# Optimization experiments

Hardware: AMD Instinct MI355X
Metric: run time of the kernel (lower is better)

The kernel has to match this reference:

```python
import math
import jax, jax.numpy as jnp
import numpy as np

D_MODEL = 1024
HEADS = 16
B, S = 4, 2048


def setup_inputs() -> dict:
    key = jax.random.key(0)
    ks = jax.random.split(key, 8)
    scale = 1.0 / math.sqrt(D_MODEL)
    return {
        "q": jax.random.normal(ks[0], (B, S, D_MODEL), dtype=jnp.float32),
        "k": jax.random.normal(ks[1], (B, S, D_MODEL), dtype=jnp.float32),
        "v": jax.random.normal(ks[2], (B, S, D_MODEL), dtype=jnp.float32),
        "mask": jax.random.randint(ks[3], (B, S), 0, 2).astype(jnp.bool_),
        "alibi_mask": jax.random.normal(ks[4], (1, HEADS, S, S), dtype=jnp.float32),
        "Wq": jax.random.normal(ks[5], (D_MODEL, D_MODEL), dtype=jnp.float32) * scale,
        "Wk": jax.random.normal(ks[6], (D_MODEL, D_MODEL), dtype=jnp.float32) * scale,
        "Wv": jax.random.normal(ks[7], (D_MODEL, D_MODEL), dtype=jnp.float32) * scale,
    }


def _split_heads(x):
    b, s, d = x.shape
    return x.reshape(b, s, HEADS, d // HEADS).transpose(0, 2, 1, 3)  # [B,H,S,hd]


def reference(q, k, v, mask, alibi_mask, Wq, Wk, Wv):
    # QKV projections (Linear, no bias)
    qh = _split_heads(q @ Wq)
    kh = _split_heads(k @ Wk)
    vh = _split_heads(v @ Wv)
    depth = qh.shape[-1]
    # naive full attention matrix [B,H,Sq,Sk]
    w = jnp.einsum("bhqd,bhkd->bhqk", qh, kh) / math.sqrt(depth)
    # mask: [B,Sk] -> [B,1,1,Sk], True = masked
    w = jnp.where(mask[:, None, None, :], -jnp.inf, w)
    w = w + alibi_mask
    a = jax.nn.softmax(w, axis=-1)  # dropout p=0 -> identity
    out = jnp.einsum("bhqk,bhkd->bhqd", a, vh)
    # combine heads -> [B,S,D]
    out = out.transpose(0, 2, 1, 3).reshape(q.shape[0], q.shape[1], -1)
    return (out, a)
```

## Files before the change

### kernel.cpp

```cpp
#include <hip/hip_runtime.h>
#include <hip/hip_bf16.h>
#include <math.h>

constexpr int B  = 4;
constexpr int S  = 2048;
constexpr int D  = 1024;
constexpr int H  = 16;
constexpr int HD = 64;
constexpr float SCALE = 0.125f;

using f32x4 = __attribute__((ext_vector_type(4))) float;
using s16x8 = __attribute__((ext_vector_type(8))) short;
using u16x8 = __attribute__((ext_vector_type(8))) unsigned short;
using u16x4 = __attribute__((ext_vector_type(4))) unsigned short;

__device__ __forceinline__ unsigned short f2bf(float f) {
    union { float f; unsigned u; } x; x.f = f;
    unsigned r = x.u + 0x7fffu + ((x.u >> 16) & 1u);
    return (unsigned short)(r >> 16);
}
__device__ __forceinline__ float bf2f(unsigned short h) {
    union { unsigned u; float f; } x; x.u = ((unsigned)h) << 16;
    return x.f;
}

#define MFMA_BF16(Af, Bf, Cf) __builtin_amdgcn_mfma_f32_16x16x32_bf16(Af, Bf, Cf, 0, 0, 0)

__global__ __launch_bounds__(256) void k_wt(const float* __restrict__ W,
                                            unsigned short* __restrict__ Wt) {
    __shared__ unsigned short T[64][68];
    const int k0 = blockIdx.x * 64, n0 = blockIdx.y * 64;
    const int t = threadIdx.x;
    {
        const int kr = t >> 4, nc4 = (t & 15) * 4;
        for (int rr = 0; rr < 4; ++rr) {
            const int kk = kr + rr * 16;
            f32x4 wv = *reinterpret_cast<const f32x4*>(&W[(size_t)(k0 + kk) * D + n0 + nc4]);
#pragma unroll
            for (int j = 0; j < 4; ++j) T[nc4 + j][kk] = f2bf(wv[j]);
        }
    }
    __syncthreads();
    {
        const int nr = t >> 4, kc4 = (t & 15) * 4;
        for (int rr = 0; rr < 4; ++rr) {
            const int nn = nr + rr * 16;
            u16x4 o;
#pragma unroll
            for (int j = 0; j < 4; ++j) o[j] = T[nn][kc4 + j];
            *reinterpret_cast<u16x4*>(&Wt[(size_t)(n0 + nn) * D + k0 + kc4]) = o;
        }
    }
}

__global__ __launch_bounds__(256) void k_proj_mfma(const float* __restrict__ X,
                                                   const unsigned short* __restrict__ Wt,
                                                   unsigned short* __restrict__ Y) {
    __shared__ alignas(16) unsigned short As[128][72];
    __shared__ alignas(16) unsigned short Bs[128][72];
    const int bm = blockIdx.y * 128, bn = blockIdx.x * 128;
    const int t = threadIdx.x, w = t >> 6, l = t & 63;
    const int wr = w >> 1, wc = w & 1;
    const int lr = l & 15, lg = l >> 4;
    f32x4 acc[4][4] = {};

    for (int k0 = 0; k0 < D; k0 += 64) {
        {
            const int c4 = (t & 15) * 4;
            int row = t >> 4;
            for (int rr = 0; rr < 8; ++rr, row += 16) {
                f32x4 xv = *reinterpret_cast<const f32x4*>(&X[(size_t)(bm + row) * D + k0 + c4]);
                u16x4 hv;
#pragma unroll
                for (int j = 0; j < 4; ++j) hv[j] = f2bf(xv[j]);
                *reinterpret_cast<u16x4*>(&As[row][c4]) = hv;
            }
        }
        for (int i = 0; i < 4; ++i) {
            const int idx = t + i * 256;
            const int row = idx >> 3, c8 = (idx & 7) * 8;
            *reinterpret_cast<u16x8*>(&Bs[row][c8]) =
                *reinterpret_cast<const u16x8*>(&Wt[(size_t)(bn + row) * D + k0 + c8]);
        }
        __syncthreads();
#pragma unroll
        for (int kk = 0; kk < 2; ++kk) {
            s16x8 af[4], bf[4];
#pragma unroll
            for (int f = 0; f < 4; ++f) {
                af[f] = *reinterpret_cast<const s16x8*>(&As[wr * 64 + f * 16 + lr][kk * 32 + lg * 8]);
                bf[f] = *reinterpret_cast<const s16x8*>(&Bs[wc * 64 + f * 16 + lr][kk * 32 + lg * 8]);
            }
#pragma unroll
            for (int fm = 0; fm < 4; ++fm)
#pragma unroll
                for (int fn = 0; fn < 4; ++fn)
                    acc[fm][fn] = MFMA_BF16(af[fm], bf[fn], acc[fm][fn]);
        }
        __syncthreads();
    }
#pragma unroll
    for (int fm = 0; fm < 4; ++fm)
#pragma unroll
        for (int fn = 0; fn < 4; ++fn)
#pragma unroll
            for (int r = 0; r < 4; ++r) {
                const int m = bm + wr * 64 + fm * 16 + lg * 4 + r;
                const int n = bn + wc * 64 + fn * 16 + lr;
                const int b = m >> 11, s = m & (S - 1);
                const int h = n >> 6, e = n & 63;
                Y[(((size_t)(b * H + h) * S) + s) * HD + e] = f2bf(acc[fm][fn][r]);
            }
}

__global__ __launch_bounds__(256) void k_vt(const unsigned short* __restrict__ Vh,
                                            unsigned short* __restrict__ VT) {
    __shared__ alignas(16) unsigned short T[64][264];
    const int bh = blockIdx.y;
    const int s0 = blockIdx.x * 256;
    const int t = threadIdx.x;
    {
        const int e4 = (t & 15) * 4;
        int sr = t >> 4;
        for (int rr = 0; rr < 16; ++rr, sr += 16) {
            u16x4 vv = *reinterpret_cast<const u16x4*>(&Vh[((size_t)bh * S + s0 + sr) * HD + e4]);
#pragma unroll
            for (int j = 0; j < 4; ++j) T[e4 + j][sr] = vv[j];
        }
    }
    __syncthreads();
    {
        const int e = t >> 2, sl0 = (t & 3) * 64;
        for (int c = 0; c < 8; ++c) {
            u16x8 o = *reinterpret_cast<const u16x8*>(&T[e][sl0 + c * 8]);
            *reinterpret_cast<u16x8*>(&VT[((size_t)bh * HD + e) * S + s0 + sl0 + c * 8]) = o;
        }
    }
}

__global__ __launch_bounds__(256) void k_abf16(const float* __restrict__ A,
                                               unsigned short* __restrict__ O) {
    const size_t N = (size_t)H * S * S;
    const size_t stride = (size_t)gridDim.x * 256 * 8;
    for (size_t i = ((size_t)blockIdx.x * 256 + threadIdx.x) * 8; i < N; i += stride) {
        f32x4 a0 = *reinterpret_cast<const f32x4*>(&A[i]);
        f32x4 a1 = *reinterpret_cast<const f32x4*>(&A[i + 4]);
        u16x8 o;
#pragma unroll
        for (int j = 0; j < 4; ++j) { o[j] = f2bf(a0[j]); o[4 + j] = f2bf(a1[j]); }
        *reinterpret_cast<u16x8*>(&O[i]) = o;
    }
}

template <bool ABF16>
__global__ __launch_bounds__(512, 4) void k_fused(
    const unsigned short* __restrict__ QH, const unsigned short* __restrict__ KH,
    const unsigned short* __restrict__ VT, const float* __restrict__ ALIBI,
    const unsigned short* __restrict__ ABF, const int* __restrict__ MASK,
    float* __restrict__ Aout, float* __restrict__ OUT) {
    __shared__ alignas(16) unsigned short Qs[128][72];
    __shared__ alignas(16) unsigned short Ks[64][72];
    __shared__ alignas(16) unsigned short Vs[64][72];
    __shared__ alignas(16) unsigned short ALs[128][72];
    __shared__ alignas(16) unsigned short Ps[128][72];

    const int bh = blockIdx.y, b = bh >> 4, h = bh & 15;
    const int q0 = blockIdx.x * 128;
    const int t = threadIdx.x, w = t >> 6, ln = t & 63;
    const int lr = ln & 15, lg = ln >> 4;
    const unsigned short NEGBIG = f2bf(-1e30f);

    const unsigned short* Qb = QH + (size_t)bh * S * HD;
    const unsigned short* Kb = KH + (size_t)bh * S * HD;
    const unsigned short* Vb = VT + (size_t)bh * HD * S;
    const size_t hoff = (size_t)h * S * S;

#pragma unroll
    for (int i = 0; i < 2; ++i) {
        const int idx = t + i * 512, row = idx >> 3, c8 = (idx & 7) * 8;
        *reinterpret_cast<u16x8*>(&Qs[row][c8]) =
            *reinterpret_cast<const u16x8*>(&Qb[(size_t)(q0 + row) * HD + c8]);
    }
    __syncthreads();
    s16x8 qf[2];
#pragma unroll
    for (int kk = 0; kk < 2; ++kk)
        qf[kk] = *reinterpret_cast<const s16x8*>(&Qs[w * 16 + lr][kk * 32 + lg * 8]);

    float psum[4] = {0.f, 0.f, 0.f, 0.f};

    for (int k0 = 0; k0 < S; k0 += 64) {
        {
            const int row = t >> 3, c8 = (t & 7) * 8;
            *reinterpret_cast<u16x8*>(&Ks[row][c8]) =
                *reinterpret_cast<const u16x8*>(&Kb[(size_t)(k0 + row) * HD + c8]);
        }
#pragma unroll
        for (int i = 0; i < 2; ++i) {
            const int idx = t + i * 512, row = idx >> 3, c8 = (idx & 7) * 8;
            int4 m0 = *reinterpret_cast<const int4*>(&MASK[b * S + k0 + c8]);
            int4 m1 = *reinterpret_cast<const int4*>(&MASK[b * S + k0 + c8 + 4]);
            u16x8 av;
            if constexpr (ABF16) {
                av = *reinterpret_cast<const u16x8*>(&ABF[hoff + (size_t)(q0 + row) * S + k0 + c8]);
            } else {
                f32x4 a0 = *reinterpret_cast<const f32x4*>(&ALIBI[hoff + (size_t)(q0 + row) * S + k0 + c8]);
                f32x4 a1 = *reinterpret_cast<const f32x4*>(&ALIBI[hoff + (size_t)(q0 + row) * S + k0 + c8 + 4]);
#pragma unroll
                for (int j = 0; j < 4; ++j) { av[j] = f2bf(a0[j]); av[4 + j] = f2bf(a1[j]); }
            }
            u16x8 sv;
            sv[0] = m0.x ? NEGBIG : av[0];
            sv[1] = m0.y ? NEGBIG : av[1];
            sv[2] = m0.z ? NEGBIG : av[2];
            sv[3] = m0.w ? NEGBIG : av[3];
            sv[4] = m1.x ? NEGBIG : av[4];
            sv[5] = m1.y ? NEGBIG : av[5];
            sv[6] = m1.z ? NEGBIG : av[6];
            sv[7] = m1.w ? NEGBIG : av[7];
            *reinterpret_cast<u16x8*>(&ALs[row][c8]) = sv;
        }
        __syncthreads();

        f32x4 acc[4] = {};
#pragma unroll
        for (int kk = 0; kk < 2; ++kk)
#pragma unroll
            for (int fn = 0; fn < 4; ++fn) {
                s16x8 kf = *reinterpret_cast<const s16x8*>(&Ks[fn * 16 + lr][kk * 32 + lg * 8]);
                acc[fn] = MFMA_BF16(qf[kk], kf, acc[fn]);
            }
#pragma unroll
        for (int r = 0; r < 4; ++r) {
            const int rowl = w * 16 + lg * 4 + r;
            float s = 0.f;
#pragma unroll
            for (int fn = 0; fn < 4; ++fn)
                s += __expf(fmaf(acc[fn][r], SCALE, bf2f(ALs[rowl][fn * 16 + lr])));
            psum[r] += s;
        }
        __syncthreads();
    }

    float invl[4];
#pragma unroll
    for (int r = 0; r < 4; ++r) {
        float ps = psum[r];
#pragma unroll
        for (int off = 1; off < 16; off <<= 1) ps += __shfl_xor(ps, off, 64);
        invl[r] = 1.0f / ps;
    }

    f32x4 oacc[4] = {};
    for (int k0 = 0; k0 < S; k0 += 64) {
        {
            const int row = t >> 3, c8 = (t & 7) * 8;
            *reinterpret_cast<u16x8*>(&Ks[row][c8]) =
                *reinterpret_cast<const u16x8*>(&Kb[(size_t)(k0 + row) * HD + c8]);
            *reinterpret_cast<u16x8*>(&Vs[row][c8]) =
                *reinterpret_cast<const u16x8*>(&Vb[(size_t)row * S + k0 + c8]);
        }
#pragma unroll
        for (int i = 0; i < 2; ++i) {
            const int idx = t + i * 512, row = idx >> 3, c8 = (idx & 7) * 8;
            int4 m0 = *reinterpret_cast<const int4*>(&MASK[b * S + k0 + c8]);
            int4 m1 = *reinterpret_cast<const int4*>(&MASK[b * S + k0 + c8 + 4]);
            u16x8 av;
            if constexpr (ABF16) {
                av = *reinterpret_cast<const u16x8*>(&ABF[hoff + (size_t)(q0 + row) * S + k0 + c8]);
            } else {
                f32x4 a0 = *reinterpret_cast<const f32x4*>(&ALIBI[hoff + (size_t)(q0 + row) * S + k0 + c8]);
                f32x4 a1 = *reinterpret_cast<const f32x4*>(&ALIBI[hoff + (size_t)(q0 + row) * S + k0 + c8 + 4]);
#pragma unroll
                for (int j = 0; j < 4; ++j) { av[j] = f2bf(a0[j]); av[4 + j] = f2bf(a1[j]); }
            }
            u16x8 sv;
            sv[0] = m0.x ? NEGBIG : av[0];
            sv[1] = m0.y ? NEGBIG : av[1];
            sv[2] = m0.z ? NEGBIG : av[2];
            sv[3] = m0.w ? NEGBIG : av[3];
            sv[4] = m1.x ? NEGBIG : av[4];
            sv[5] = m1.y ? NEGBIG : av[5];
            sv[6] = m1.z ? NEGBIG : av[6];
            sv[7] = m1.w ? NEGBIG : av[7];
            *reinterpret_cast<u16x8*>(&ALs[row][c8]) = sv;
        }
        __syncthreads();

        f32x4 acc[4] = {};
#pragma unroll
        for (int kk = 0; kk < 2; ++kk)
#pragma unroll
            for (int fn = 0; fn < 4; ++fn) {
                s16x8 kf = *reinterpret_cast<const s16x8*>(&Ks[fn * 16 + lr][kk * 32 + lg * 8]);
                acc[fn] = MFMA_BF16(qf[kk], kf, acc[fn]);
            }
#pragma unroll
        for (int r = 0; r < 4; ++r) {
            const int rowl = w * 16 + lg * 4 + r;
#pragma unroll
            for (int fn = 0; fn < 4; ++fn) {
                float p = __expf(fmaf(acc[fn][r], SCALE, bf2f(ALs[rowl][fn * 16 + lr]))) * invl[r];
                Ps[rowl][fn * 16 + lr] = f2bf(p);
            }
        }
        __syncthreads();

#pragma unroll
        for (int i = 0; i < 2; ++i) {
            const int idx = t + i * 512, row = idx >> 3, sub = idx & 7;
            u16x8 pv = *reinterpret_cast<const u16x8*>(&Ps[row][sub * 8]);
            f32x4 o0, o1;
#pragma unroll
            for (int j = 0; j < 4; ++j) { o0[j] = bf2f(pv[j]); o1[j] = bf2f(pv[4 + j]); }
            float* dst = &Aout[((size_t)bh * S + q0 + row) * S + k0 + sub * 8];
            *reinterpret_cast<f32x4*>(dst) = o0;
            *reinterpret_cast<f32x4*>(dst + 4) = o1;
        }
#pragma unroll
        for (int c = 0; c < 2; ++c) {
            s16x8 pa = *reinterpret_cast<const s16x8*>(&Ps[w * 16 + lr][c * 32 + lg * 8]);
#pragma unroll
            for (int fn = 0; fn < 4; ++fn) {
                s16x8 vf = *reinterpret_cast<const s16x8*>(&Vs[fn * 16 + lr][c * 32 + lg * 8]);
                oacc[fn] = MFMA_BF16(pa, vf, oacc[fn]);
            }
        }
        __syncthreads();
    }

#pragma unroll
    for (int fn = 0; fn < 4; ++fn)
#pragma unroll
        for (int r = 0; r < 4; ++r)
            OUT[(size_t)(b * S + q0 + w * 16 + lg * 4 + r) * D + h * HD + fn * 16 + lr] =
                oacc[fn][r];
}

extern "C" void kernel_launch(void* const* d_in, const int* in_sizes, int n_in,
                              void* d_out, int out_size, void* d_ws, size_t ws_size,
                              hipStream_t stream) {
    const float* q     = (const float*)d_in[0];
    const float* k     = (const float*)d_in[1];
    const float* v     = (const float*)d_in[2];
    const int*   mask  = (const int*)d_in[3];
    const float* alibi = (const float*)d_in[4];
    const float* Wq    = (const float*)d_in[5];
    const float* Wk    = (const float*)d_in[6];
    const float* Wv    = (const float*)d_in[7];

    float* out = (float*)d_out;
    float* a   = out + (size_t)B * S * D;

    const size_t NH = (size_t)B * H * S * HD;
    unsigned short* qh  = (unsigned short*)d_ws;
    unsigned short* kh  = qh + NH;
    unsigned short* vh  = kh + NH;
    unsigned short* vT  = vh + NH;
    unsigned short* wqt = vT + NH;
    unsigned short* wkt = wqt + (size_t)D * D;
    unsigned short* wvt = wkt + (size_t)D * D;
    unsigned short* abf = wvt + (size_t)D * D;

    const size_t need_bf16 = ((size_t)(abf - qh) + (size_t)H * S * S) * sizeof(unsigned short);
    const bool use_abf16 = ws_size >= need_bf16;

    const dim3 blk(256);

    k_wt<<<dim3(D / 64, D / 64), blk, 0, stream>>>(Wq, wqt);
    k_wt<<<dim3(D / 64, D / 64), blk, 0, stream>>>(Wk, wkt);
    k_wt<<<dim3(D / 64, D / 64), blk, 0, stream>>>(Wv, wvt);

    if (use_abf16)
        k_abf16<<<dim3(8192), blk, 0, stream>>>(alibi, abf);

    k_proj_mfma<<<dim3(D / 128, (B * S) / 128), blk, 0, stream>>>(q, wqt, qh);
    k_proj_mfma<<<dim3(D / 128, (B * S) / 128), blk, 0, stream>>>(k, wkt, kh);
    k_proj_mfma<<<dim3(D / 128, (B * S) / 128), blk, 0, stream>>>(v, wvt, vh);

    k_vt<<<dim3(S / 256, B * H), blk, 0, stream>>>(vh, vT);

    if (use_abf16)
        k_fused<true><<<dim3(S / 128, B * H), dim3(512), 0, stream>>>(
            qh, kh, vT, alibi, abf, mask, a, out);
    else
        k_fused<false><<<dim3(S / 128, B * H), dim3(512), 0, stream>>>(
            qh, kh, vT, alibi, abf, mask, a, out);
}
```

Baseline: 714.3 us.

## Split fused attention into sum-exp and output kernels with per-column mask add

The single fused kernel is split into two launches: one computes the softmax denominators and writes inverse row sums to a workspace buffer, and the other recomputes scores, writes the probability matrix and accumulates the output. Each kernel uses less LDS (no Q tile; the sum kernel also drops the V and P tiles) and loads Q fragments straight from global memory. Masking changes from per-element selects while staging the alibi tile to a per-lane additive term read once per column. The intent is to raise occupancy and cut LDS and staging work, at the cost of an extra launch and a small global round trip for the inverse sums.

After: 714.3 us. No clear change (-0.0%).

```diff
diff --git a/kernel.cpp b/kernel.cpp
--- a/kernel.cpp
+++ b/kernel.cpp
@@ -153,39 +153,27 @@
 }
 
 template <bool ABF16>
-__global__ __launch_bounds__(512, 4) void k_fused(
+__global__ __launch_bounds__(512, 4) void k_sumexp(
     const unsigned short* __restrict__ QH, const unsigned short* __restrict__ KH,
-    const unsigned short* __restrict__ VT, const float* __restrict__ ALIBI,
-    const unsigned short* __restrict__ ABF, const int* __restrict__ MASK,
-    float* __restrict__ Aout, float* __restrict__ OUT) {
-    __shared__ alignas(16) unsigned short Qs[128][72];
+    const float* __restrict__ ALIBI, const unsigned short* __restrict__ ABF,
+    const int* __restrict__ MASK, float* __restrict__ INVL) {
     __shared__ alignas(16) unsigned short Ks[64][72];
-    __shared__ alignas(16) unsigned short Vs[64][72];
     __shared__ alignas(16) unsigned short ALs[128][72];
-    __shared__ alignas(16) unsigned short Ps[128][72];
 
     const int bh = blockIdx.y, b = bh >> 4, h = bh & 15;
     const int q0 = blockIdx.x * 128;
     const int t = threadIdx.x, w = t >> 6, ln = t & 63;
     const int lr = ln & 15, lg = ln >> 4;
-    const unsigned short NEGBIG = f2bf(-1e30f);
 
     const unsigned short* Qb = QH + (size_t)bh * S * HD;
     const unsigned short* Kb = KH + (size_t)bh * S * HD;
-    const unsigned short* Vb = VT + (size_t)bh * HD * S;
     const size_t hoff = (size_t)h * S * S;
 
-#pragma unroll
-    for (int i = 0; i < 2; ++i) {
-        const int idx = t + i * 512, row = idx >> 3, c8 = (idx & 7) * 8;
-        *reinterpret_cast<u16x8*>(&Qs[row][c8]) =
-            *reinterpret_cast<const u16x8*>(&Qb[(size_t)(q0 + row) * HD + c8]);
-    }
-    __syncthreads();
     s16x8 qf[2];
 #pragma unroll
     for (int kk = 0; kk < 2; ++kk)
-        qf[kk] = *reinterpret_cast<const s16x8*>(&Qs[w * 16 + lr][kk * 32 + lg * 8]);
+        qf[kk] = *reinterpret_cast<const s16x8*>(
+            &Qb[(size_t)(q0 + w * 16 + lr) * HD + kk * 32 + lg * 8]);
 
     float psum[4] = {0.f, 0.f, 0.f, 0.f};
 
@@ -198,8 +186,6 @@
 #pragma unroll
         for (int i = 0; i < 2; ++i) {
             const int idx = t + i * 512, row = idx >> 3, c8 = (idx & 7) * 8;
-            int4 m0 = *reinterpret_cast<const int4*>(&MASK[b * S + k0 + c8]);
-            int4 m1 = *reinterpret_cast<const int4*>(&MASK[b * S + k0 + c8 + 4]);
             u16x8 av;
             if constexpr (ABF16) {
                 av = *reinterpret_cast<const u16x8*>(&ABF[hoff + (size_t)(q0 + row) * S + k0 + c8]);
@@ -209,17 +195,12 @@
 #pragma unroll
                 for (int j = 0; j < 4; ++j) { av[j] = f2bf(a0[j]); av[4 + j] = f2bf(a1[j]); }
             }
-            u16x8 sv;
-            sv[0] = m0.x ? NEGBIG : av[0];
-            sv[1] = m0.y ? NEGBIG : av[1];
-            sv[2] = m0.z ? NEGBIG : av[2];
-            sv[3] = m0.w ? NEGBIG : av[3];
-            sv[4] = m1.x ? NEGBIG : av[4];
-            sv[5] = m1.y ? NEGBIG : av[5];
-            sv[6] = m1.z ? NEGBIG : av[6];
-            sv[7] = m1.w ? NEGBIG : av[7];
-            *reinterpret_cast<u16x8*>(&ALs[row][c8]) = sv;
-        }
+            *reinterpret_cast<u16x8*>(&ALs[row][c8]) = av;
+        }
+        float madd[4];
+#pragma unroll
+        for (int fn = 0; fn < 4; ++fn)
+            madd[fn] = MASK[b * S + k0 + fn * 16 + lr] ? -1e30f : 0.f;
         __syncthreads();
 
         f32x4 acc[4] = {};
@@ -236,20 +217,54 @@
             float s = 0.f;
 #pragma unroll
             for (int fn = 0; fn < 4; ++fn)
-                s += __expf(fmaf(acc[fn][r], SCALE, bf2f(ALs[rowl][fn * 16 + lr])));
+                s += __expf(fmaf(acc[fn][r], SCALE, bf2f(ALs[rowl][fn * 16 + lr]) + madd[fn]));
             psum[r] += s;
         }
         __syncthreads();
     }
 
-    float invl[4];
 #pragma unroll
     for (int r = 0; r < 4; ++r) {
         float ps = psum[r];
 #pragma unroll
         for (int off = 1; off < 16; off <<= 1) ps += __shfl_xor(ps, off, 64);
-        invl[r] = 1.0f / ps;
-    }
+        if (lr == 0)
+            INVL[(size_t)bh * S + q0 + w * 16 + lg * 4 + r] = 1.0f / ps;
+    }
+}
+
+template <bool ABF16>
+__global__ __launch_bounds__(512, 2) void k_attn(
+    const unsigned short* __restrict__ QH, const unsigned short* __restrict__ KH,
+    const unsigned short* __restrict__ VT, const float* __restrict__ ALIBI,
+    const unsigned short* __restrict__ ABF, const int* __restrict__ MASK,
+    const float* __restrict__ INVL, float* __restrict__ Aout,
+    float* __restrict__ OUT) {
+    __shared__ alignas(16) unsigned short Ps[128][72];
+    __shared__ alignas(16) unsigned short Ks[64][72];
+    __shared__ alignas(16) unsigned short Vs[64][72];
+    __shared__ alignas(16) unsigned short ALs[128][72];
+
+    const int bh = blockIdx.y, b = bh >> 4, h = bh & 15;
+    const int q0 = blockIdx.x * 128;
+    const int t = threadIdx.x, w = t >> 6, ln = t & 63;
+    const int lr = ln & 15, lg = ln >> 4;
+
+    const unsigned short* Qb = QH + (size_t)bh * S * HD;
+    const unsigned short* Kb = KH + (size_t)bh * S * HD;
+    const unsigned short* Vb = VT + (size_t)bh * HD * S;
+    const size_t hoff = (size_t)h * S * S;
+
+    s16x8 qf[2];
+#pragma unroll
+    for (int kk = 0; kk < 2; ++kk)
+        qf[kk] = *reinterpret_cast<const s16x8*>(
+            &Qb[(size_t)(q0 + w * 16 + lr) * HD + kk * 32 + lg * 8]);
+
+    float invl[4];
+#pragma unroll
+    for (int r = 0; r < 4; ++r)
+        invl[r] = INVL[(size_t)bh * S + q0 + w * 16 + lg * 4 + r];
 
     f32x4 oacc[4] = {};
     for (int k0 = 0; k0 < S; k0 += 64) {
@@ -263,8 +278,6 @@
 #pragma unroll
         for (int i = 0; i < 2; ++i) {
             const int idx = t + i * 512, row = idx >> 3, c8 = (idx & 7) * 8;
-            int4 m0 = *reinterpret_cast<const int4*>(&MASK[b * S + k0 + c8]);
-            int4 m1 = *reinterpret_cast<const int4*>(&MASK[b * S + k0 + c8 + 4]);
             u16x8 av;
             if constexpr (ABF16) {
                 av = *reinterpret_cast<const u16x8*>(&ABF[hoff + (size_t)(q0 + row) * S + k0 + c8]);
@@ -274,17 +287,12 @@
 #pragma unroll
                 for (int j = 0; j < 4; ++j) { av[j] = f2bf(a0[j]); av[4 + j] = f2bf(a1[j]); }
             }
-            u16x8 sv;
-            sv[0] = m0.x ? NEGBIG : av[0];
-            sv[1] = m0.y ? NEGBIG : av[1];
-            sv[2] = m0.z ? NEGBIG : av[2];
-            sv[3] = m0.w ? NEGBIG : av[3];
-            sv[4] = m1.x ? NEGBIG : av[4];
-            sv[5] = m1.y ? NEGBIG : av[5];
-            sv[6] = m1.z ? NEGBIG : av[6];
-            sv[7] = m1.w ? NEGBIG : av[7];
-            *reinterpret_cast<u16x8*>(&ALs[row][c8]) = sv;
-        }
+            *reinterpret_cast<u16x8*>(&ALs[row][c8]) = av;
+        }
+        float madd[4];
+#pragma unroll
+        for (int fn = 0; fn < 4; ++fn)
+            madd[fn] = MASK[b * S + k0 + fn * 16 + lr] ? -1e30f : 0.f;
         __syncthreads();
 
         f32x4 acc[4] = {};
@@ -300,7 +308,8 @@
             const int rowl = w * 16 + lg * 4 + r;
 #pragma unroll
             for (int fn = 0; fn < 4; ++fn) {
-                float p = __expf(fmaf(acc[fn][r], SCALE, bf2f(ALs[rowl][fn * 16 + lr]))) * invl[r];
+                float p = __expf(fmaf(acc[fn][r], SCALE,
+                                      bf2f(ALs[rowl][fn * 16 + lr]) + madd[fn])) * invl[r];
                 Ps[rowl][fn * 16 + lr] = f2bf(p);
             }
         }
@@ -360,9 +369,11 @@
     unsigned short* wqt = vT + NH;
     unsigned short* wkt = wqt + (size_t)D * D;
     unsigned short* wvt = wkt + (size_t)D * D;
-    unsigned short* abf = wvt + (size_t)D * D;
-
-    const size_t need_bf16 = ((size_t)(abf - qh) + (size_t)H * S * S) * sizeof(unsigned short);
+    float*          invl = (float*)(wvt + (size_t)D * D);
+    unsigned short* abf  = (unsigned short*)(invl + (size_t)B * H * S);
+
+    const size_t need_bf16 =
+        ((size_t)((unsigned short*)abf - qh) + (size_t)H * S * S) * sizeof(unsigned short);
     const bool use_abf16 = ws_size >= need_bf16;
 
     const dim3 blk(256);
@@ -380,10 +391,15 @@
 
     k_vt<<<dim3(S / 256, B * H), blk, 0, stream>>>(vh, vT);
 
-    if (use_abf16)
-        k_fused<true><<<dim3(S / 128, B * H), dim3(512), 0, stream>>>(
-            qh, kh, vT, alibi, abf, mask, a, out);
-    else
-        k_fused<false><<<dim3(S / 128, B * H), dim3(512), 0, stream>>>(
-            qh, kh, vT, alibi, abf, mask, a, out);
-}
+    if (use_abf16) {
+        k_sumexp<true><<<dim3(S / 128, B * H), dim3(512), 0, stream>>>(
+            qh, kh, alibi, abf, mask, invl);
+        k_attn<true><<<dim3(S / 128, B * H), dim3(512), 0, stream>>>(
+            qh, kh, vT, alibi, abf, mask, invl, a, out);
+    } else {
+        k_sumexp<false><<<dim3(S / 128, B * H), dim3(512), 0, stream>>>(
+            qh, kh, alibi, abf, mask, invl);
+        k_attn<false><<<dim3(S / 128, B * H), dim3(512), 0, stream>>>(
+            qh, kh, vT, alibi, abf, mask, invl, a, out);
+    }
+}
```
